# Optimization experiments

Hardware: AMD Instinct MI355X
Metric: run time of the kernel (lower is better)

The kernel has to match this reference:

```python
import jax, jax.numpy as jnp
import numpy as np

PI_APPROX = 3.1415926  # the source uses 3.1415926, not math.pi
N_RINGS = 10
N_ANGLES = 36  # k in range(0, 360, 10)


def setup_inputs() -> dict:
    key = jax.random.key(0)
    k1, k2, k3 = jax.random.split(key, 3)
    B, N = 32, 16384
    pred = jax.random.normal(k1, (B, N_RINGS), dtype=jnp.float32)
    target = jax.random.normal(k2, (B, N, 3), dtype=jnp.float32)
    trans_feat = jax.random.normal(k3, (B, 256), dtype=jnp.float32)
    return {"pred": pred, "target": target, "trans_feat": trans_feat}


def _generate_points(pred):
    # pred: [B, 10] radii. For ring j: center = [0.04, 0.15*j - 0.7, 0.0],
    # axis = y, firstPoint (centered) = [-r, 0, 0]. Rotating about y by angle a:
    # R @ [-r,0,0] = [-r*cos(a), 0, r*sin(a)]; then add center back.
    B = pred.shape[0]
    j = jnp.arange(N_RINGS, dtype=pred.dtype)
    cy = 0.15 * j - 0.7                                   # [10]
    ang = jnp.arange(0, 360, 10, dtype=pred.dtype) * (2.0 * PI_APPROX / 360.0)  # [36]
    c, s = jnp.cos(ang), jnp.sin(ang)
    r = pred[:, :, None]                                  # [B,10,1]
    px = -r * c[None, None, :] + 0.04                     # [B,10,36]
    py = jnp.broadcast_to(cy[None, :, None], px.shape)    # [B,10,36]
    pz = r * s[None, None, :]                             # [B,10,36]
    pts = jnp.stack([px, py, pz], axis=-1)                # [B,10,36,3]
    return pts.reshape(B, N_RINGS * N_ANGLES, 3)          # [B,360,3]


def reference(pred, target, trans_feat):
    B = pred.shape[0]
    pts = _generate_points(pred.reshape(B, N_RINGS))      # [B,360,3]
    # squared pairwise distances via ||a||^2 + ||b||^2 - 2 a.b
    d2 = (jnp.sum(pts * pts, axis=-1)[:, :, None]
          + jnp.sum(target * target, axis=-1)[:, None, :]
          - 2.0 * jnp.einsum('bpd,bnd->bpn', pts, target))  # [B,360,N]
    d2 = jnp.maximum(d2, 0.0)
    # original: min over target of ||pt - tgt||, then squared == min of squared dist
    min_d2 = jnp.min(d2, axis=-1)                         # [B,360]
    return jnp.mean(min_d2)
```

## Files before the change

### kernel.cpp

```cpp
#include <hip/hip_runtime.h>
#include <math.h>
#include <float.h>

#define N_RINGS  10
#define N_ANGLES 36
#define NP       360
#define PI_APPROX 3.1415926f

#define BLOCK  512
#define WPB    8
#define CHUNK  1024
#define PPT    6

typedef float v2f __attribute__((ext_vector_type(2)));

__global__ __launch_bounds__(BLOCK) void chamfer_partial(
    const float* __restrict__ pred,
    const float* __restrict__ target,
    float* __restrict__ part,
    int N, int chunks)
{
    __shared__ v2f   tp[CHUNK / 2][4];
    __shared__ float pm[WPB * NP];
    __shared__ float cs_c[N_ANGLES], cs_s[N_ANGLES];

    const int b   = blockIdx.x / chunks;
    const int cg  = blockIdx.x % chunks;
    const int n0  = cg * CHUNK;
    const int tid = threadIdx.x;
    const int cnt = min(CHUNK, N - n0);
    const int cntp = (cnt + 1) & ~1;

    if (tid < N_ANGLES) {
        float angf = (float)(10 * tid) * (2.0f * PI_APPROX / 360.0f);
        double ang = (double)angf;
        cs_c[tid] = (float)cos(ang);
        cs_s[tid] = (float)sin(ang);
    }
    for (int i = tid; i < cntp; i += BLOCK) {
        int ii = min(i, cnt - 1);
        const float* t = target + ((size_t)b * N + (size_t)(n0 + ii)) * 3;
        float x = t[0], y = t[1], z = t[2];
        int j = i >> 1, h = i & 1;
        tp[j][0][h] = x;
        tp[j][1][h] = y;
        tp[j][2][h] = z;
        tp[j][3][h] = x * x + y * y + z * z;
    }
    __syncthreads();

    const int lane = tid & 63;
    const int w    = tid >> 6;

    float qx[PPT], qy[PPT], qz[PPT], pp2[PPT], m[PPT];
    #pragma unroll
    for (int k = 0; k < PPT; ++k) {
        int s = lane + 64 * k;
        int j = s / N_ANGLES;
        int a = s - j * N_ANGLES;
        int jc = (j < N_RINGS) ? j : (N_RINGS - 1);
        float r  = pred[b * N_RINGS + jc];
        float px = -r * cs_c[a] + 0.04f;
        float py = 0.15f * (float)jc - 0.7f;
        float pz = r * cs_s[a];
        pp2[k] = px * px + py * py + pz * pz;
        qx[k] = -2.0f * px;
        qy[k] = -2.0f * py;
        qz[k] = -2.0f * pz;
        m[k]  = FLT_MAX;
    }

    const int pairs = cntp >> 1;
    #pragma unroll 4
    for (int k = w; k < pairs; k += WPB) {
        v2f xv = tp[k][0], yv = tp[k][1], zv = tp[k][2], wv = tp[k][3];
        #pragma unroll
        for (int i = 0; i < PPT; ++i) {
            v2f h = qz[i] * zv + wv;
            h = qy[i] * yv + h;
            h = qx[i] * xv + h;
            m[i] = fminf(m[i], fminf(h.x, h.y));
        }
    }

    #pragma unroll
    for (int k = 0; k < PPT; ++k) {
        int s = lane + 64 * k;
        if (s < NP) pm[w * NP + s] = fmaxf(pp2[k] + m[k], 0.0f);
    }
    __syncthreads();

    for (int p = tid; p < NP; p += BLOCK) {
        float v = pm[p];
        #pragma unroll
        for (int ww = 1; ww < WPB; ++ww)
            v = fminf(v, pm[ww * NP + p]);
        part[((size_t)b * chunks + cg) * NP + p] = v;
    }
}

__global__ __launch_bounds__(256) void batch_sum(
    const float* __restrict__ part, double* __restrict__ ws2,
    int chunks)
{
    __shared__ double sd[4];
    const int b   = blockIdx.x;
    const int tid = threadIdx.x;
    const float* pb = part + (size_t)b * chunks * NP;

    double s = 0.0;
    for (int p = tid; p < NP; p += 256) {
        float mn = pb[p];
        for (int c = 1; c < chunks; ++c)
            mn = fminf(mn, pb[(size_t)c * NP + p]);
        s += (double)mn;
    }
    #pragma unroll
    for (int off = 32; off > 0; off >>= 1)
        s += __shfl_down(s, off, 64);
    if ((tid & 63) == 0) sd[tid >> 6] = s;
    __syncthreads();
    if (tid == 0)
        ws2[b] = sd[0] + sd[1] + sd[2] + sd[3];
}

__global__ __launch_bounds__(64) void final_mean(
    const double* __restrict__ ws2, float* __restrict__ out, int B)
{
    const int tid = threadIdx.x;
    double s = (tid < B) ? ws2[tid] : 0.0;
    #pragma unroll
    for (int off = 32; off > 0; off >>= 1)
        s += __shfl_down(s, off, 64);
    if (tid == 0)
        out[0] = (float)(s / (double)(B * NP));
}

extern "C" void kernel_launch(void* const* d_in, const int* in_sizes, int n_in,
                              void* d_out, int out_size, void* d_ws, size_t ws_size,
                              hipStream_t stream) {
    const float* pred   = (const float*)d_in[0];
    const float* target = (const float*)d_in[1];

    const int B = in_sizes[0] / N_RINGS;
    const int N = in_sizes[1] / (3 * B);
    const int chunks = (N + CHUNK - 1) / CHUNK;

    float* part = (float*)d_ws;
    size_t partBytes = (size_t)B * chunks * NP * sizeof(float);
    double* ws2 = (double*)((char*)d_ws + partBytes);
    float* out = (float*)d_out;

    hipLaunchKernelGGL(chamfer_partial, dim3(B * chunks), dim3(BLOCK), 0, stream,
                       pred, target, part, N, chunks);
    hipLaunchKernelGGL(batch_sum, dim3(B), dim3(256), 0, stream,
                       part, ws2, chunks);
    hipLaunchKernelGGL(final_mean, dim3(1), dim3(64), 0, stream,
                       ws2, out, B);
}
```

Before: 86.86 us.

## Precompute target pairs and query points in a separate prep kernel

Adds a prep kernel that converts the target points into an SoA paired layout with precomputed squared norms, and computes the 360 query points per batch into a global float4 buffer. The main kernel then reads target pairs directly from global memory with wave-uniform indexing instead of staging them through LDS, and it no longer does any trig work. This adds one kernel launch and a full extra write and read of a workspace larger than the target array. It also drops the LDS staging barrier, at the cost of per-wave global loads inside the inner loop.

```diff
diff --git a/kernel.cpp b/kernel.cpp
--- a/kernel.cpp
+++ b/kernel.cpp
@@ -14,66 +14,83 @@
 
 typedef float v2f __attribute__((ext_vector_type(2)));
 
-__global__ __launch_bounds__(BLOCK) void chamfer_partial(
+__global__ __launch_bounds__(256) void prep(
     const float* __restrict__ pred,
     const float* __restrict__ target,
+    v2f*  __restrict__ tpairs,
+    float4* __restrict__ pts4,
+    int N, int B)
+{
+    const int gid = blockIdx.x * blockDim.x + threadIdx.x;
+    const int halfN = N >> 1;
+    const int pairsTot = B * halfN;
+
+    if (gid < pairsTot) {
+        int bp = gid / halfN;
+        int pr = gid - bp * halfN;
+        const float* t = target + ((size_t)bp * N + 2 * (size_t)pr) * 3;
+        float x0 = t[0], y0 = t[1], z0 = t[2];
+        float x1 = t[3], y1 = t[4], z1 = t[5];
+        v2f* o = tpairs + (size_t)gid * 4;
+        o[0] = (v2f){x0, x1};
+        o[1] = (v2f){y0, y1};
+        o[2] = (v2f){z0, z1};
+        o[3] = (v2f){x0 * x0 + y0 * y0 + z0 * z0,
+                     x1 * x1 + y1 * y1 + z1 * z1};
+    }
+    if (gid < B * NP) {
+        int bb = gid / NP;
+        int p  = gid - bb * NP;
+        int j  = p / N_ANGLES;
+        int a  = p - j * N_ANGLES;
+        float angf = (float)(10 * a) * (2.0f * PI_APPROX / 360.0f);
+        double ang = (double)angf;
+        float c = (float)cos(ang), s = (float)sin(ang);
+        float r  = pred[bb * N_RINGS + j];
+        float px = -r * c + 0.04f;
+        float py = 0.15f * (float)j - 0.7f;
+        float pz = r * s;
+        pts4[gid] = make_float4(-2.0f * px, -2.0f * py, -2.0f * pz,
+                                px * px + py * py + pz * pz);
+    }
+}
+
+__global__ __launch_bounds__(BLOCK) void chamfer_partial(
+    const float4* __restrict__ pts4,
+    const v2f*  __restrict__ tpairs,
     float* __restrict__ part,
     int N, int chunks)
 {
-    __shared__ v2f   tp[CHUNK / 2][4];
     __shared__ float pm[WPB * NP];
-    __shared__ float cs_c[N_ANGLES], cs_s[N_ANGLES];
 
     const int b   = blockIdx.x / chunks;
     const int cg  = blockIdx.x % chunks;
-    const int n0  = cg * CHUNK;
     const int tid = threadIdx.x;
-    const int cnt = min(CHUNK, N - n0);
-    const int cntp = (cnt + 1) & ~1;
+    const int lane = tid & 63;
+    const int wu  = __builtin_amdgcn_readfirstlane(tid >> 6);
 
-    if (tid < N_ANGLES) {
-        float angf = (float)(10 * tid) * (2.0f * PI_APPROX / 360.0f);
-        double ang = (double)angf;
-        cs_c[tid] = (float)cos(ang);
-        cs_s[tid] = (float)sin(ang);
-    }
-    for (int i = tid; i < cntp; i += BLOCK) {
-        int ii = min(i, cnt - 1);
-        const float* t = target + ((size_t)b * N + (size_t)(n0 + ii)) * 3;
-        float x = t[0], y = t[1], z = t[2];
-        int j = i >> 1, h = i & 1;
-        tp[j][0][h] = x;
-        tp[j][1][h] = y;
-        tp[j][2][h] = z;
-        tp[j][3][h] = x * x + y * y + z * z;
-    }
-    __syncthreads();
+    const int halfN = N >> 1;
+    const int pairsChunk = CHUNK >> 1;
+    const int kend = min(pairsChunk, halfN - cg * pairsChunk);
+    const v2f* tpb = tpairs + ((size_t)b * halfN + (size_t)cg * pairsChunk) * 4;
 
-    const int lane = tid & 63;
-    const int w    = tid >> 6;
-
-    float qx[PPT], qy[PPT], qz[PPT], pp2[PPT], m[PPT];
+    float qx[PPT], qy[PPT], qz[PPT], pw[PPT], m[PPT];
     #pragma unroll
     for (int k = 0; k < PPT; ++k) {
-        int s = lane + 64 * k;
-        int j = s / N_ANGLES;
-        int a = s - j * N_ANGLES;
-        int jc = (j < N_RINGS) ? j : (N_RINGS - 1);
-        float r  = pred[b * N_RINGS + jc];
-        float px = -r * cs_c[a] + 0.04f;
-        float py = 0.15f * (float)jc - 0.7f;
-        float pz = r * cs_s[a];
-        pp2[k] = px * px + py * py + pz * pz;
-        qx[k] = -2.0f * px;
-        qy[k] = -2.0f * py;
-        qz[k] = -2.0f * pz;
-        m[k]  = FLT_MAX;
+        int s  = lane + 64 * k;
+        int sc = (s < NP) ? s : (NP - 1);
+        float4 q = pts4[b * NP + sc];
+        qx[k] = q.x; qy[k] = q.y; qz[k] = q.z; pw[k] = q.w;
+        m[k] = FLT_MAX;
     }
 
-    const int pairs = cntp >> 1;
     #pragma unroll 4
-    for (int k = w; k < pairs; k += WPB) {
-        v2f xv = tp[k][0], yv = tp[k][1], zv = tp[k][2], wv = tp[k][3];
+    for (int k = wu; k < kend; k += WPB) {
+        int base = 4 * k;
+        v2f xv = tpb[base + 0];
+        v2f yv = tpb[base + 1];
+        v2f zv = tpb[base + 2];
+        v2f wv = tpb[base + 3];
         #pragma unroll
         for (int i = 0; i < PPT; ++i) {
             v2f h = qz[i] * zv + wv;
@@ -86,7 +103,7 @@
     #pragma unroll
     for (int k = 0; k < PPT; ++k) {
         int s = lane + 64 * k;
-        if (s < NP) pm[w * NP + s] = fmaxf(pp2[k] + m[k], 0.0f);
+        if (s < NP) pm[wu * NP + s] = fmaxf(pw[k] + m[k], 0.0f);
     }
     __syncthreads();
 
@@ -145,14 +162,22 @@
     const int B = in_sizes[0] / N_RINGS;
     const int N = in_sizes[1] / (3 * B);
     const int chunks = (N + CHUNK - 1) / CHUNK;
+    const int halfN  = N >> 1;
 
-    float* part = (float*)d_ws;
+    v2f* tpairs = (v2f*)d_ws;
+    size_t tpairsBytes = (size_t)B * halfN * 4 * sizeof(v2f);
+    float4* pts4 = (float4*)((char*)d_ws + tpairsBytes);
+    size_t pts4Bytes = (size_t)B * NP * sizeof(float4);
+    float* part = (float*)((char*)d_ws + tpairsBytes + pts4Bytes);
     size_t partBytes = (size_t)B * chunks * NP * sizeof(float);
-    double* ws2 = (double*)((char*)d_ws + partBytes);
+    double* ws2 = (double*)((char*)d_ws + tpairsBytes + pts4Bytes + partBytes);
     float* out = (float*)d_out;
 
+    const int prepThreads = B * halfN;
+    hipLaunchKernelGGL(prep, dim3((prepThreads + 255) / 256), dim3(256), 0, stream,
+                       pred, target, tpairs, pts4, N, B);
     hipLaunchKernelGGL(chamfer_partial, dim3(B * chunks), dim3(BLOCK), 0, stream,
-                       pred, target, part, N, chunks);
+                       pts4, tpairs, part, N, chunks);
     hipLaunchKernelGGL(batch_sum, dim3(B), dim3(256), 0, stream,
                        part, ws2, chunks);
     hipLaunchKernelGGL(final_mean, dim3(1), dim3(64), 0, stream,
```

Result: slower. 95.86 us (+10.4%).
